# Kernel optimization log

Measured on AMD Instinct MI355X. Metric: run time of the kernel, lower is better.

Reference implementation:

```python
import jax, jax.numpy as jnp
import numpy as np

N = 50000      # nodes
E = 800000     # edges (avg degree 16)
H = 128        # hidden
ED = 64        # edge_dim
L = 3          # num_layers
LN_EPS = 1e-5


def setup_inputs() -> dict:
    key = jax.random.key(0)
    ks = jax.random.split(key, 12)
    s = jax.random.normal(ks[0], (N, H), dtype=jnp.float32)
    edge_index = jax.random.randint(ks[1], (2, E), 0, N, dtype=jnp.int32)
    edge_attr = jax.random.normal(ks[2], (E, ED), dtype=jnp.float32)
    sc = 0.02
    We = sc * jax.random.normal(ks[3], (L, ED, H), dtype=jnp.float32)
    be = sc * jax.random.normal(ks[4], (L, H), dtype=jnp.float32)
    W1 = sc * jax.random.normal(ks[5], (L, H, H), dtype=jnp.float32)
    b1 = sc * jax.random.normal(ks[6], (L, H), dtype=jnp.float32)
    W2 = sc * jax.random.normal(ks[7], (L, H, H), dtype=jnp.float32)
    b2 = sc * jax.random.normal(ks[8], (L, H), dtype=jnp.float32)
    gamma = jnp.ones((L, H), dtype=jnp.float32)
    beta = jnp.zeros((L, H), dtype=jnp.float32)
    return {"s": s, "edge_index": edge_index, "edge_attr": edge_attr,
            "We": We, "be": be, "W1": W1, "b1": b1, "W2": W2, "b2": b2,
            "gamma": gamma, "beta": beta}


def reference(s, edge_index, edge_attr, We, be, W1, b1, W2, b2, gamma, beta):
    src = edge_index[0]  # j (source of message)
    dst = edge_index[1]  # i (target / aggregation index)
    for l in range(L):
        # GINEConv: message = relu(x_j + Lin(edge_attr)); sum-aggregate; eps=0
        e = edge_attr @ We[l] + be[l]                       # [E, H]
        msg = jax.nn.relu(s[src] + e)                       # [E, H] gather + fuse
        agg = jax.ops.segment_sum(msg, dst, num_segments=N)  # [N, H] scatter-add
        h = s + agg                                         # (1+eps)*x + aggr, eps=0
        h = jax.nn.silu(h @ W1[l] + b1[l]) @ W2[l] + b2[l]   # GINE MLP
        s = s + h                                           # residual
        mu = jnp.mean(s, axis=-1, keepdims=True)
        var = jnp.var(s, axis=-1, keepdims=True)
        s = (s - mu) * jax.lax.rsqrt(var + LN_EPS) * gamma[l] + beta[l]
        s = jax.nn.silu(s)
        # dropout p=0.0 / eval mode -> identity
    return s
```

## Files before the change

kernel.cpp:

```cpp
#include <hip/hip_runtime.h>
#include <hip/hip_bf16.h>

#define HH 128
#define EDD 64
#define NLAYER 3
#define LN_EPS 1e-5f
#define LROW 136

typedef __attribute__((ext_vector_type(8))) __bf16 bf16x8;
typedef __attribute__((ext_vector_type(4))) float f32x4;

static __device__ __forceinline__ float bf2f(unsigned short u) {
    return __uint_as_float(((unsigned)u) << 16);
}
static __device__ __forceinline__ unsigned short f2bf(float f) {
    return __builtin_bit_cast(unsigned short, (__bf16)f);
}
static __device__ __forceinline__ float silu(float x) {
    return x / (1.f + __expf(-x));
}

__global__ __launch_bounds__(256) void hist_kernel(
    const int* __restrict__ dst, int* __restrict__ cnt, int E)
{
    for (int e = blockIdx.x * blockDim.x + threadIdx.x; e < E;
         e += gridDim.x * blockDim.x)
        atomicAdd(&cnt[dst[e]], 1);
}

__global__ __launch_bounds__(1024) void scan_kernel(
    const int* __restrict__ cnt, int* __restrict__ off, int N)
{
    __shared__ int ls[1024];
    const int t = threadIdx.x;
    const int C = (N + 1023) >> 10;
    const int lo = t * C;
    const int hi = min(lo + C, N);
    int sum = 0;
    for (int i = lo; i < hi; ++i) sum += cnt[i];
    ls[t] = sum;
    __syncthreads();
    for (int d = 1; d < 1024; d <<= 1) {
        int v = (t >= d) ? ls[t - d] : 0;
        __syncthreads();
        ls[t] += v;
        __syncthreads();
    }
    int excl = (t == 0) ? 0 : ls[t - 1];
    for (int i = lo; i < hi; ++i) { off[i] = excl; excl += cnt[i]; }
    if (t == 1023) off[N] = ls[1023];
}

__global__ __launch_bounds__(256) void scatter2_kernel(
    const int* __restrict__ src, const int* __restrict__ dst,
    int* __restrict__ cursor, int* __restrict__ src_s,
    int* __restrict__ eid_s, int E)
{
    if (blockIdx.x == 0 && threadIdx.x < 16) {
        src_s[E + threadIdx.x] = 0;
        eid_s[E + threadIdx.x] = 0;
    }
    for (int e = blockIdx.x * blockDim.x + threadIdx.x; e < E;
         e += gridDim.x * blockDim.x) {
        const int pos = atomicAdd(&cursor[dst[e]], 1);
        src_s[pos] = src[e];
        eid_s[pos] = e;
    }
}

__global__ __launch_bounds__(256) void conv_ea(
    const float* __restrict__ ea, unsigned short* __restrict__ ea_b,
    long long total4)
{
    for (long long i = blockIdx.x * 256LL + threadIdx.x; i < total4;
         i += gridDim.x * 256LL) {
        const float4 v = reinterpret_cast<const float4*>(ea)[i];
        ushort4 o;
        o.x = f2bf(v.x); o.y = f2bf(v.y); o.z = f2bf(v.z); o.w = f2bf(v.w);
        reinterpret_cast<ushort4*>(ea_b)[i] = o;
    }
}

__global__ __launch_bounds__(256) void conv_s(
    const float* __restrict__ s0, unsigned int* __restrict__ sbp,
    long long total4)
{
    for (long long i = blockIdx.x * 256LL + threadIdx.x; i < total4;
         i += gridDim.x * 256LL) {
        const float4 v = reinterpret_cast<const float4*>(s0)[i];
        const unsigned a = (unsigned)f2bf(v.x) | ((unsigned)f2bf(v.y) << 16);
        const unsigned b = (unsigned)f2bf(v.z) | ((unsigned)f2bf(v.w) << 16);
        reinterpret_cast<uint2*>(sbp)[i] = make_uint2(a, b);
    }
}

__global__ void prep_we(const float* __restrict__ We, bf16x8* __restrict__ WeB)
{
    const int t = blockIdx.x * blockDim.x + threadIdx.x;
    if (t >= NLAYER * 16 * 64) return;
    const int lane  = t & 63;
    const int frag  = (t >> 6) & 15;
    const int layer = t >> 10;
    const int kt = frag >> 3, ct = frag & 7;
    const int col = ct * 16 + (lane & 15);
    const int k0  = kt * 32 + (lane >> 4) * 8;
    bf16x8 v;
    #pragma unroll
    for (int j = 0; j < 8; ++j)
        v[j] = (__bf16)We[(long long)layer * EDD * HH + (k0 + j) * HH + col];
    WeB[t] = v;
}

__global__ void prep_w128(const float* __restrict__ W, bf16x8* __restrict__ WB)
{
    const int t = blockIdx.x * blockDim.x + threadIdx.x;
    if (t >= NLAYER * 32 * 64) return;
    const int lane  = t & 63;
    const int frag  = (t >> 6) & 31;
    const int layer = t >> 11;
    const int kt = frag >> 3, ct = frag & 7;
    const int col = ct * 16 + (lane & 15);
    const int k0  = kt * 32 + (lane >> 4) * 8;
    bf16x8 v;
    #pragma unroll
    for (int j = 0; j < 8; ++j)
        v[j] = (__bf16)W[(long long)layer * HH * HH + (k0 + j) * HH + col];
    WB[t] = v;
}

__global__ __launch_bounds__(256, 3) void gine_agg_mfma(
    const float* __restrict__ s,
    const unsigned short* __restrict__ sb,
    const int* __restrict__ src_s,
    const int* __restrict__ eid_s,
    const int* __restrict__ off,
    const unsigned short* __restrict__ ea_b,
    const bf16x8* __restrict__ WeB,
    const float* __restrict__ be,
    unsigned short* __restrict__ hb16,
    int N, int E)
{
    __shared__ unsigned short lsb[2][16 * LROW];

    const int tid  = threadIdx.x;
    const int wave = tid >> 6;
    const int half = wave & 1;
    const int slot = wave >> 1;
    const int lane = tid & 63;
    const int lmod = lane & 15;
    const int ldiv = lane >> 4;

    bf16x8 wb0[4], wb1[4];
    #pragma unroll
    for (int c = 0; c < 4; ++c) {
        wb0[c] = WeB[(0 * 8 + half * 4 + c) * 64 + lane];
        wb1[c] = WeB[(1 * 8 + half * 4 + c) * 64 + lane];
    }
    float bev[4];
    #pragma unroll
    for (int c = 0; c < 4; ++c) bev[c] = be[(half * 4 + c) * 16 + lmod];

    const int st_slot = tid >> 7;
    const int st_row  = (tid >> 3) & 15;
    const int st_su   = (tid & 7) * 16;

    for (int base = blockIdx.x * 2; base < N; base += gridDim.x * 2) {
        const int n0 = base;
        const int n1 = (base + 1 < N) ? base + 1 : base;
        const int q0 = off[n0], q0e = off[n0 + 1];
        const int q1 = off[n1], q1e = off[n1 + 1];
        const int iters = max((q0e - q0 + 15) >> 4, (q1e - q1 + 15) >> 4);

        const int myn = slot ? n1 : n0;
        const int p0  = slot ? q1 : q0;
        const int p1  = slot ? q1e : q0e;
        const int sp0 = st_slot ? q1 : q0;

        float acc[4] = {0.f, 0.f, 0.f, 0.f};

        int snode = src_s[min(sp0 + st_row, E + 15)];
        const unsigned short* srow0 = &sb[(long long)snode * HH + st_su];
        uint4 sva = *reinterpret_cast<const uint4*>(srow0);
        uint4 svb = *reinterpret_cast<const uint4*>(srow0 + 8);
        int rowid = eid_s[min(p0 + lmod, E + 15)];
        const unsigned short* ar0 = ea_b + (long long)rowid * EDD + ldiv * 8;
        bf16x8 a0 = *reinterpret_cast<const bf16x8*>(ar0);
        bf16x8 a1 = *reinterpret_cast<const bf16x8*>(ar0 + 32);

        for (int it = 0; it < iters; ++it) {
            __syncthreads();
            unsigned short* drow = &lsb[st_slot][st_row * LROW + st_su];
            *reinterpret_cast<uint4*>(drow)     = sva;
            *reinterpret_cast<uint4*>(drow + 8) = svb;

            uint4 nva = sva, nvb = svb;
            bf16x8 na0 = a0, na1 = a1;
            if (it + 1 < iters) {
                const int ns = src_s[min(sp0 + (it + 1) * 16 + st_row, E + 15)];
                const unsigned short* nsr = &sb[(long long)ns * HH + st_su];
                nva = *reinterpret_cast<const uint4*>(nsr);
                nvb = *reinterpret_cast<const uint4*>(nsr + 8);
                const int nr = eid_s[min(p0 + (it + 1) * 16 + lmod, E + 15)];
                const unsigned short* nar = ea_b + (long long)nr * EDD + ldiv * 8;
                na0 = *reinterpret_cast<const bf16x8*>(nar);
                na1 = *reinterpret_cast<const bf16x8*>(nar + 32);
            }

            f32x4 cf[4];
            #pragma unroll
            for (int c = 0; c < 4; ++c) {
                f32x4 z = {0.f, 0.f, 0.f, 0.f};
                z = __builtin_amdgcn_mfma_f32_16x16x32_bf16(a0, wb0[c], z, 0, 0, 0);
                z = __builtin_amdgcn_mfma_f32_16x16x32_bf16(a1, wb1[c], z, 0, 0, 0);
                cf[c] = z;
            }

            __syncthreads();

            const int rem = p1 - (p0 + it * 16);
            #pragma unroll
            for (int r = 0; r < 4; ++r) {
                if (ldiv * 4 + r < rem) {
                    const unsigned short* lr = &lsb[slot][(ldiv * 4 + r) * LROW];
                    #pragma unroll
                    for (int c = 0; c < 4; ++c)
                        acc[c] += fmaxf(
                            bf2f(lr[(half * 4 + c) * 16 + lmod]) + cf[c][r] + bev[c],
                            0.f);
                }
            }

            sva = nva; svb = nvb; a0 = na0; a1 = na1;
        }

        #pragma unroll
        for (int c = 0; c < 4; ++c) {
            acc[c] += __shfl_xor(acc[c], 16, 64);
            acc[c] += __shfl_xor(acc[c], 32, 64);
        }
        const float av = (ldiv == 0) ? acc[0] : (ldiv == 1) ? acc[1]
                       : (ldiv == 2) ? acc[2] : acc[3];
        const int col = (half * 4 + ldiv) * 16 + lmod;
        const long long nb = (long long)myn * HH;
        hb16[nb + col] = f2bf(s[nb + col] + av);
    }
}

__global__ __launch_bounds__(256) void gine_mlp(
    const float* __restrict__ s_in,
    const unsigned short* __restrict__ h16,
    const bf16x8* __restrict__ W1B, const float* __restrict__ b1,
    const bf16x8* __restrict__ W2B, const float* __restrict__ b2,
    const float* __restrict__ gamma, const float* __restrict__ beta,
    float* __restrict__ s_out,
    unsigned short* __restrict__ sb_out,
    int N)
{
    __shared__ unsigned short t1t[16 * LROW];
    __shared__ float2 red[4][16];

    const int wave = threadIdx.x >> 6;
    const int lane = threadIdx.x & 63;
    const int lmod = lane & 15;
    const int ldiv = lane >> 4;

    bf16x8 wf1[4][2], wf2[4][2];
    #pragma unroll
    for (int kt = 0; kt < 4; ++kt) {
        wf1[kt][0] = W1B[(kt * 8 + 2 * wave    ) * 64 + lane];
        wf1[kt][1] = W1B[(kt * 8 + 2 * wave + 1) * 64 + lane];
        wf2[kt][0] = W2B[(kt * 8 + 2 * wave    ) * 64 + lane];
        wf2[kt][1] = W2B[(kt * 8 + 2 * wave + 1) * 64 + lane];
    }
    float4 b1v[2], b2v[2], gv[2], ev[2];
    #pragma unroll
    for (int ctl = 0; ctl < 2; ++ctl) {
        const int oc0 = (2 * wave + ctl) * 16 + ldiv * 4;
        b1v[ctl] = *reinterpret_cast<const float4*>(&b1[oc0]);
        b2v[ctl] = *reinterpret_cast<const float4*>(&b2[oc0]);
        gv[ctl]  = *reinterpret_cast<const float4*>(&gamma[oc0]);
        ev[ctl]  = *reinterpret_cast<const float4*>(&beta[oc0]);
    }

    const int ntiles = (N + 15) >> 4;
    for (int t = blockIdx.x; t < ntiles; t += gridDim.x) {
        const int node = t * 16 + lmod;
        const long long nb = (long long)min(node, N - 1) * HH;

        f32x4 c0 = {0.f, 0.f, 0.f, 0.f};
        f32x4 c1 = {0.f, 0.f, 0.f, 0.f};
        #pragma unroll
        for (int kt = 0; kt < 4; ++kt) {
            const bf16x8 hf = *reinterpret_cast<const bf16x8*>(
                &h16[nb + kt * 32 + ldiv * 8]);
            c0 = __builtin_amdgcn_mfma_f32_16x16x32_bf16(wf1[kt][0], hf, c0, 0, 0, 0);
            c1 = __builtin_amdgcn_mfma_f32_16x16x32_bf16(wf1[kt][1], hf, c1, 0, 0, 0);
        }
        #pragma unroll
        for (int ctl = 0; ctl < 2; ++ctl) {
            const f32x4 cc = ctl ? c1 : c0;
            const float4 bb = ctl ? b1v[1] : b1v[0];
            uint2 pk;
            pk.x = (unsigned)f2bf(silu(cc[0] + bb.x)) |
                   ((unsigned)f2bf(silu(cc[1] + bb.y)) << 16);
            pk.y = (unsigned)f2bf(silu(cc[2] + bb.z)) |
                   ((unsigned)f2bf(silu(cc[3] + bb.w)) << 16);
            const int oc0 = (2 * wave + ctl) * 16 + ldiv * 4;
            *reinterpret_cast<uint2*>(&t1t[lmod * LROW + oc0]) = pk;
        }
        __syncthreads();

        f32x4 d0 = {0.f, 0.f, 0.f, 0.f};
        f32x4 d1 = {0.f, 0.f, 0.f, 0.f};
        #pragma unroll
        for (int kt = 0; kt < 4; ++kt) {
            const bf16x8 tf = *reinterpret_cast<const bf16x8*>(
                &t1t[lmod * LROW + kt * 32 + ldiv * 8]);
            d0 = __builtin_amdgcn_mfma_f32_16x16x32_bf16(wf2[kt][0], tf, d0, 0, 0, 0);
            d1 = __builtin_amdgcn_mfma_f32_16x16x32_bf16(wf2[kt][1], tf, d1, 0, 0, 0);
        }

        float v[2][4];
        float sum = 0.f, ssq = 0.f;
        #pragma unroll
        for (int ctl = 0; ctl < 2; ++ctl) {
            const int oc0 = (2 * wave + ctl) * 16 + ldiv * 4;
            const float4 sv = *reinterpret_cast<const float4*>(&s_in[nb + oc0]);
            const f32x4 dd = ctl ? d1 : d0;
            const float4 bb = ctl ? b2v[1] : b2v[0];
            v[ctl][0] = sv.x + dd[0] + bb.x;
            v[ctl][1] = sv.y + dd[1] + bb.y;
            v[ctl][2] = sv.z + dd[2] + bb.z;
            v[ctl][3] = sv.w + dd[3] + bb.w;
            #pragma unroll
            for (int r = 0; r < 4; ++r) { sum += v[ctl][r]; ssq += v[ctl][r] * v[ctl][r]; }
        }
        sum += __shfl_xor(sum, 16, 64); sum += __shfl_xor(sum, 32, 64);
        ssq += __shfl_xor(ssq, 16, 64); ssq += __shfl_xor(ssq, 32, 64);
        if (ldiv == 0) red[wave][lmod] = make_float2(sum, ssq);
        __syncthreads();
        float ts = 0.f, tq = 0.f;
        #pragma unroll
        for (int w = 0; w < 4; ++w) {
            const float2 rr = red[w][lmod];
            ts += rr.x; tq += rr.y;
        }
        __syncthreads();

        const float mu = ts * (1.0f / HH);
        const float var = tq * (1.0f / HH) - mu * mu;
        const float rs = rsqrtf(var + LN_EPS);

        if (node < N) {
            #pragma unroll
            for (int ctl = 0; ctl < 2; ++ctl) {
                const int oc0 = (2 * wave + ctl) * 16 + ldiv * 4;
                float o[4];
                o[0] = silu((v[ctl][0] - mu) * rs * gv[ctl].x + ev[ctl].x);
                o[1] = silu((v[ctl][1] - mu) * rs * gv[ctl].y + ev[ctl].y);
                o[2] = silu((v[ctl][2] - mu) * rs * gv[ctl].z + ev[ctl].z);
                o[3] = silu((v[ctl][3] - mu) * rs * gv[ctl].w + ev[ctl].w);
                *reinterpret_cast<float4*>(&s_out[nb + oc0]) =
                    make_float4(o[0], o[1], o[2], o[3]);
                uint2 pk;
                pk.x = (unsigned)f2bf(o[0]) | ((unsigned)f2bf(o[1]) << 16);
                pk.y = (unsigned)f2bf(o[2]) | ((unsigned)f2bf(o[3]) << 16);
                *reinterpret_cast<uint2*>(&sb_out[nb + oc0]) = pk;
            }
        }
    }
}

extern "C" void kernel_launch(void* const* d_in, const int* in_sizes, int n_in,
                              void* d_out, int out_size, void* d_ws, size_t ws_size,
                              hipStream_t stream) {
    const float* s0  = (const float*)d_in[0];
    const int*   ei  = (const int*)  d_in[1];
    const float* ea  = (const float*)d_in[2];
    const float* We  = (const float*)d_in[3];
    const float* be  = (const float*)d_in[4];
    const float* W1  = (const float*)d_in[5];
    const float* b1  = (const float*)d_in[6];
    const float* W2  = (const float*)d_in[7];
    const float* b2  = (const float*)d_in[8];
    const float* gm  = (const float*)d_in[9];
    const float* bt  = (const float*)d_in[10];

    const int NH = in_sizes[0];
    const int N  = NH / HH;
    const int E  = in_sizes[1] / 2;
    const int* src = ei;
    const int* dst = ei + E;

    float*          sbuf  = (float*)d_ws;
    unsigned short* sb    = (unsigned short*)(sbuf + NH);
    unsigned short* hb16  = sb + NH;
    unsigned short* ea_b  = hb16 + NH;
    bf16x8*         WeB   = (bf16x8*)(ea_b + (size_t)E * EDD);
    bf16x8*         W1B   = WeB + NLAYER * 16 * 64;
    bf16x8*         W2B   = W1B + NLAYER * 32 * 64;
    int*            src_s = (int*)(W2B + NLAYER * 32 * 64);
    int*            eid_s = src_s + (E + 16);
    int*            off   = eid_s + (E + 16);
    int*            cursor= off + (N + 1);

    hipMemsetAsync(cursor, 0, sizeof(int) * N, stream);
    hist_kernel<<<1024, 256, 0, stream>>>(dst, cursor, E);
    scan_kernel<<<1, 1024, 0, stream>>>(cursor, off, N);
    hipMemcpyAsync(cursor, off, sizeof(int) * N, hipMemcpyDeviceToDevice, stream);
    scatter2_kernel<<<1024, 256, 0, stream>>>(src, dst, cursor, src_s, eid_s, E);
    conv_ea<<<2048, 256, 0, stream>>>(ea, ea_b, (long long)E * EDD / 4);
    conv_s<<<1024, 256, 0, stream>>>(s0, (unsigned int*)sb, (long long)NH / 4);
    prep_we<<<12, 256, 0, stream>>>(We, WeB);
    prep_w128<<<24, 256, 0, stream>>>(W1, W1B);
    prep_w128<<<24, 256, 0, stream>>>(W2, W2B);

    for (int l = 0; l < NLAYER; ++l) {
        const float* scur = (l == 0) ? s0 : sbuf;
        gine_agg_mfma<<<4096, 256, 0, stream>>>(scur, sb, src_s, eid_s, off, ea_b,
                                                WeB + (size_t)l * 16 * 64,
                                                be + l * HH, hb16, N, E);
        float* sout = (l == NLAYER - 1) ? (float*)d_out : sbuf;
        gine_mlp<<<2048, 256, 0, stream>>>(scur, hb16,
                                           W1B + (size_t)l * 32 * 64, b1 + l * HH,
                                           W2B + (size_t)l * 32 * 64, b2 + l * HH,
                                           gm + l * HH, bt + l * HH,
                                           sout, sb, N);
    }
}
```

Before: 611.8 us.

## Pre-sort edge attributes by destination and keep node state in bf16 only

Scatter now records each edge's sorted position, and the edge-attribute conversion writes bf16 rows directly in destination-sorted order. The aggregation kernel can then stream edge features contiguously instead of gathering through an edge-id indirection. The fp32 node-state buffer is dropped: the residual is read from the bf16 copy, and fp32 output is written only in the last layer. The scan also initialises the cursor in place, which removes a device memcpy. The trade-off is lower precision in the residual path and an extra scattered write pass during preprocessing.

```diff
diff --git a/kernel.cpp b/kernel.cpp
--- a/kernel.cpp
+++ b/kernel.cpp
@@ -29,7 +29,7 @@
 }
 
 __global__ __launch_bounds__(1024) void scan_kernel(
-    const int* __restrict__ cnt, int* __restrict__ off, int N)
+    int* __restrict__ cnt_cursor, int* __restrict__ off, int N)
 {
     __shared__ int ls[1024];
     const int t = threadIdx.x;
@@ -37,7 +37,7 @@
     const int lo = t * C;
     const int hi = min(lo + C, N);
     int sum = 0;
-    for (int i = lo; i < hi; ++i) sum += cnt[i];
+    for (int i = lo; i < hi; ++i) sum += cnt_cursor[i];
     ls[t] = sum;
     __syncthreads();
     for (int d = 1; d < 1024; d <<= 1) {
@@ -47,37 +47,40 @@
         __syncthreads();
     }
     int excl = (t == 0) ? 0 : ls[t - 1];
-    for (int i = lo; i < hi; ++i) { off[i] = excl; excl += cnt[i]; }
+    for (int i = lo; i < hi; ++i) {
+        const int c = cnt_cursor[i];
+        off[i] = excl;
+        cnt_cursor[i] = excl;
+        excl += c;
+    }
     if (t == 1023) off[N] = ls[1023];
 }
 
-__global__ __launch_bounds__(256) void scatter2_kernel(
+__global__ __launch_bounds__(256) void scatter3_kernel(
     const int* __restrict__ src, const int* __restrict__ dst,
     int* __restrict__ cursor, int* __restrict__ src_s,
-    int* __restrict__ eid_s, int E)
-{
-    if (blockIdx.x == 0 && threadIdx.x < 16) {
+    int* __restrict__ pos_e, int E)
+{
+    if (blockIdx.x == 0 && threadIdx.x < 16)
         src_s[E + threadIdx.x] = 0;
-        eid_s[E + threadIdx.x] = 0;
-    }
     for (int e = blockIdx.x * blockDim.x + threadIdx.x; e < E;
          e += gridDim.x * blockDim.x) {
         const int pos = atomicAdd(&cursor[dst[e]], 1);
         src_s[pos] = src[e];
-        eid_s[pos] = e;
-    }
-}
-
-__global__ __launch_bounds__(256) void conv_ea(
-    const float* __restrict__ ea, unsigned short* __restrict__ ea_b,
-    long long total4)
-{
-    for (long long i = blockIdx.x * 256LL + threadIdx.x; i < total4;
-         i += gridDim.x * 256LL) {
-        const float4 v = reinterpret_cast<const float4*>(ea)[i];
-        ushort4 o;
-        o.x = f2bf(v.x); o.y = f2bf(v.y); o.z = f2bf(v.z); o.w = f2bf(v.w);
-        reinterpret_cast<ushort4*>(ea_b)[i] = o;
+        pos_e[e] = pos;
+    }
+}
+
+__global__ __launch_bounds__(256) void conv_ea_sorted(
+    const float* __restrict__ ea, const int* __restrict__ pos_e,
+    unsigned short* __restrict__ ea_s, int E)
+{
+    const int wave = threadIdx.x >> 6;
+    const int lane = threadIdx.x & 63;
+    for (int e = blockIdx.x * 4 + wave; e < E; e += gridDim.x * 4) {
+        const float v = ea[(long long)e * EDD + lane];
+        const int pos = pos_e[e];
+        ea_s[(long long)pos * EDD + lane] = f2bf(v);
     }
 }
 
@@ -129,12 +132,10 @@
 }
 
 __global__ __launch_bounds__(256, 3) void gine_agg_mfma(
-    const float* __restrict__ s,
     const unsigned short* __restrict__ sb,
     const int* __restrict__ src_s,
-    const int* __restrict__ eid_s,
     const int* __restrict__ off,
-    const unsigned short* __restrict__ ea_b,
+    const unsigned short* __restrict__ ea_s,
     const bf16x8* __restrict__ WeB,
     const float* __restrict__ be,
     unsigned short* __restrict__ hb16,
@@ -178,12 +179,11 @@
 
         float acc[4] = {0.f, 0.f, 0.f, 0.f};
 
-        int snode = src_s[min(sp0 + st_row, E + 15)];
+        int snode = src_s[sp0 + st_row];
         const unsigned short* srow0 = &sb[(long long)snode * HH + st_su];
         uint4 sva = *reinterpret_cast<const uint4*>(srow0);
         uint4 svb = *reinterpret_cast<const uint4*>(srow0 + 8);
-        int rowid = eid_s[min(p0 + lmod, E + 15)];
-        const unsigned short* ar0 = ea_b + (long long)rowid * EDD + ldiv * 8;
+        const unsigned short* ar0 = ea_s + (long long)(p0 + lmod) * EDD + ldiv * 8;
         bf16x8 a0 = *reinterpret_cast<const bf16x8*>(ar0);
         bf16x8 a1 = *reinterpret_cast<const bf16x8*>(ar0 + 32);
 
@@ -196,12 +196,12 @@
             uint4 nva = sva, nvb = svb;
             bf16x8 na0 = a0, na1 = a1;
             if (it + 1 < iters) {
-                const int ns = src_s[min(sp0 + (it + 1) * 16 + st_row, E + 15)];
+                const int ns = src_s[sp0 + (it + 1) * 16 + st_row];
                 const unsigned short* nsr = &sb[(long long)ns * HH + st_su];
                 nva = *reinterpret_cast<const uint4*>(nsr);
                 nvb = *reinterpret_cast<const uint4*>(nsr + 8);
-                const int nr = eid_s[min(p0 + (it + 1) * 16 + lmod, E + 15)];
-                const unsigned short* nar = ea_b + (long long)nr * EDD + ldiv * 8;
+                const unsigned short* nar =
+                    ea_s + (long long)(p0 + (it + 1) * 16 + lmod) * EDD + ldiv * 8;
                 na0 = *reinterpret_cast<const bf16x8*>(nar);
                 na1 = *reinterpret_cast<const bf16x8*>(nar + 32);
             }
@@ -242,17 +242,17 @@
                        : (ldiv == 2) ? acc[2] : acc[3];
         const int col = (half * 4 + ldiv) * 16 + lmod;
         const long long nb = (long long)myn * HH;
-        hb16[nb + col] = f2bf(s[nb + col] + av);
+        hb16[nb + col] = f2bf(bf2f(sb[nb + col]) + av);
     }
 }
 
 __global__ __launch_bounds__(256) void gine_mlp(
-    const float* __restrict__ s_in,
+    const unsigned short* __restrict__ sb_in,
     const unsigned short* __restrict__ h16,
     const bf16x8* __restrict__ W1B, const float* __restrict__ b1,
     const bf16x8* __restrict__ W2B, const float* __restrict__ b2,
     const float* __restrict__ gamma, const float* __restrict__ beta,
-    float* __restrict__ s_out,
+    float* __restrict__ fout,
     unsigned short* __restrict__ sb_out,
     int N)
 {
@@ -325,13 +325,13 @@
         #pragma unroll
         for (int ctl = 0; ctl < 2; ++ctl) {
             const int oc0 = (2 * wave + ctl) * 16 + ldiv * 4;
-            const float4 sv = *reinterpret_cast<const float4*>(&s_in[nb + oc0]);
+            const ushort4 sv = *reinterpret_cast<const ushort4*>(&sb_in[nb + oc0]);
             const f32x4 dd = ctl ? d1 : d0;
             const float4 bb = ctl ? b2v[1] : b2v[0];
-            v[ctl][0] = sv.x + dd[0] + bb.x;
-            v[ctl][1] = sv.y + dd[1] + bb.y;
-            v[ctl][2] = sv.z + dd[2] + bb.z;
-            v[ctl][3] = sv.w + dd[3] + bb.w;
+            v[ctl][0] = bf2f(sv.x) + dd[0] + bb.x;
+            v[ctl][1] = bf2f(sv.y) + dd[1] + bb.y;
+            v[ctl][2] = bf2f(sv.z) + dd[2] + bb.z;
+            v[ctl][3] = bf2f(sv.w) + dd[3] + bb.w;
             #pragma unroll
             for (int r = 0; r < 4; ++r) { sum += v[ctl][r]; ssq += v[ctl][r] * v[ctl][r]; }
         }
@@ -360,12 +360,13 @@
                 o[1] = silu((v[ctl][1] - mu) * rs * gv[ctl].y + ev[ctl].y);
                 o[2] = silu((v[ctl][2] - mu) * rs * gv[ctl].z + ev[ctl].z);
                 o[3] = silu((v[ctl][3] - mu) * rs * gv[ctl].w + ev[ctl].w);
-                *reinterpret_cast<float4*>(&s_out[nb + oc0]) =
-                    make_float4(o[0], o[1], o[2], o[3]);
                 uint2 pk;
                 pk.x = (unsigned)f2bf(o[0]) | ((unsigned)f2bf(o[1]) << 16);
                 pk.y = (unsigned)f2bf(o[2]) | ((unsigned)f2bf(o[3]) << 16);
                 *reinterpret_cast<uint2*>(&sb_out[nb + oc0]) = pk;
+                if (fout)
+                    *reinterpret_cast<float4*>(&fout[nb + oc0]) =
+                        make_float4(o[0], o[1], o[2], o[3]);
             }
         }
     }
@@ -392,39 +393,37 @@
     const int* src = ei;
     const int* dst = ei + E;
 
-    float*          sbuf  = (float*)d_ws;
-    unsigned short* sb    = (unsigned short*)(sbuf + NH);
+    unsigned short* sb    = (unsigned short*)d_ws;
     unsigned short* hb16  = sb + NH;
-    unsigned short* ea_b  = hb16 + NH;
-    bf16x8*         WeB   = (bf16x8*)(ea_b + (size_t)E * EDD);
+    unsigned short* ea_s  = hb16 + NH;
+    bf16x8*         WeB   = (bf16x8*)(ea_s + (size_t)(E + 16) * EDD);
     bf16x8*         W1B   = WeB + NLAYER * 16 * 64;
     bf16x8*         W2B   = W1B + NLAYER * 32 * 64;
     int*            src_s = (int*)(W2B + NLAYER * 32 * 64);
-    int*            eid_s = src_s + (E + 16);
-    int*            off   = eid_s + (E + 16);
+    int*            pos_e = src_s + (E + 16);
+    int*            off   = pos_e + E;
     int*            cursor= off + (N + 1);
 
     hipMemsetAsync(cursor, 0, sizeof(int) * N, stream);
     hist_kernel<<<1024, 256, 0, stream>>>(dst, cursor, E);
     scan_kernel<<<1, 1024, 0, stream>>>(cursor, off, N);
-    hipMemcpyAsync(cursor, off, sizeof(int) * N, hipMemcpyDeviceToDevice, stream);
-    scatter2_kernel<<<1024, 256, 0, stream>>>(src, dst, cursor, src_s, eid_s, E);
-    conv_ea<<<2048, 256, 0, stream>>>(ea, ea_b, (long long)E * EDD / 4);
+    scatter3_kernel<<<1024, 256, 0, stream>>>(src, dst, cursor, src_s, pos_e, E);
+    conv_ea_sorted<<<2048, 256, 0, stream>>>(ea, pos_e, ea_s, E);
     conv_s<<<1024, 256, 0, stream>>>(s0, (unsigned int*)sb, (long long)NH / 4);
     prep_we<<<12, 256, 0, stream>>>(We, WeB);
     prep_w128<<<24, 256, 0, stream>>>(W1, W1B);
     prep_w128<<<24, 256, 0, stream>>>(W2, W2B);
 
+    const int ntiles = (N + 15) >> 4;
     for (int l = 0; l < NLAYER; ++l) {
-        const float* scur = (l == 0) ? s0 : sbuf;
-        gine_agg_mfma<<<4096, 256, 0, stream>>>(scur, sb, src_s, eid_s, off, ea_b,
+        gine_agg_mfma<<<4096, 256, 0, stream>>>(sb, src_s, off, ea_s,
                                                 WeB + (size_t)l * 16 * 64,
                                                 be + l * HH, hb16, N, E);
-        float* sout = (l == NLAYER - 1) ? (float*)d_out : sbuf;
-        gine_mlp<<<2048, 256, 0, stream>>>(scur, hb16,
-                                           W1B + (size_t)l * 32 * 64, b1 + l * HH,
-                                           W2B + (size_t)l * 32 * 64, b2 + l * HH,
-                                           gm + l * HH, bt + l * HH,
-                                           sout, sb, N);
-    }
-}
+        float* fout = (l == NLAYER - 1) ? (float*)d_out : nullptr;
+        gine_mlp<<<ntiles, 256, 0, stream>>>(sb, hb16,
+                                             W1B + (size_t)l * 32 * 64, b1 + l * HH,
+                                             W2B + (size_t)l * 32 * 64, b2 + l * HH,
+                                             gm + l * HH, bt + l * HH,
+                                             fout, sb, N);
+    }
+}
```

Result: no change. 623.5 us (+1.9%).
